# Kernel tuning notes

Measured on AMD Instinct MI355X. Metric: run time of the kernel, lower is better.

The kernel has to match this reference:

```python
import jax, jax.numpy as jnp
import numpy as np

N_EMBD = 2048
N_HEAD = 16
HEAD_DIM = N_EMBD // N_HEAD  # 128
ROPE_BASE = 10000.0


def _rope_cos_sin(T, dim, dtype):
    theta = 1.0 / (ROPE_BASE ** (jnp.arange(0, dim, 2, dtype=jnp.float32) / dim))  # [dim/2]
    freqs = jnp.arange(T, dtype=jnp.float32)[:, None] * theta[None, :]  # [T, dim/2]
    return jnp.cos(freqs).astype(dtype), jnp.sin(freqs).astype(dtype)


def _apply_rope(t, cos, sin):
    # t: [B,H,T,D]; interleaved (even, odd) pairs form complex numbers.
    B, H, T, D = t.shape
    tr = t.reshape(B, H, T, D // 2, 2)
    a, b = tr[..., 0], tr[..., 1]
    # (a + ib) * (cos + i sin)
    out = jnp.stack([a * cos - b * sin, a * sin + b * cos], axis=-1)
    return out.reshape(B, H, T, D)


def setup_inputs() -> dict:
    key = jax.random.key(0)
    k1, k2, k3 = jax.random.split(key, 3)
    B, T, C = 2, 2048, N_EMBD
    s = 1.0 / np.sqrt(C)
    return {
        "x": jax.random.normal(k1, (B, T, C), dtype=jnp.float32),
        "w_att": jax.random.normal(k2, (3 * C, C), dtype=jnp.float32) * s,
        "b_att": jnp.zeros((3 * C,), dtype=jnp.float32),
        "w_proj": jax.random.normal(k3, (C, C), dtype=jnp.float32) * s,
        "b_proj": jnp.zeros((C,), dtype=jnp.float32),
    }


def reference(x, w_att, b_att, w_proj, b_proj):
    B, T, C = x.shape
    H, D = N_HEAD, HEAD_DIM
    qkv = x @ w_att.T + b_att  # [B,T,3C]
    q, k, v = jnp.split(qkv, 3, axis=-1)
    # [B,T,C] -> [B,H,T,D]
    q, k, v = (t.reshape(B, T, H, D).transpose(0, 2, 1, 3) for t in (q, k, v))
    cos, sin = _rope_cos_sin(T, D, jnp.float32)  # [T, D/2]
    cos = cos[None, None]  # [1,1,T,D/2]
    sin = sin[None, None]
    q = _apply_rope(q, cos, sin)
    k = _apply_rope(k, cos, sin)
    # causal SDPA
    scale = 1.0 / np.sqrt(D)
    scores = jnp.einsum('bhqd,bhkd->bhqk', q, k) * scale
    mask = jnp.tril(jnp.ones((T, T), dtype=bool))
    scores = jnp.where(mask, scores, jnp.finfo(scores.dtype).min)
    attn = jax.nn.softmax(scores, axis=-1)
    y = jnp.einsum('bhqk,bhkd->bhqd', attn, v)  # [B,H,T,D]
    y = y.transpose(0, 2, 1, 3).reshape(B, T, C)
    return y @ w_proj.T + b_proj
```

## Files before the change

kernel.cpp:

```cpp
#include <hip/hip_runtime.h>
#include <hip/hip_bf16.h>
#include <math.h>

#define DEVI __device__ __forceinline__

typedef __attribute__((ext_vector_type(8))) short bf16x8;
typedef __attribute__((ext_vector_type(4))) float f32x4;

constexpr int Bn = 2;
constexpr int Tn = 2048;
constexpr int Cn = 2048;
constexpr int Hn = 16;
constexpr int Dn = 128;
constexpr int Mrows = Bn * Tn;
constexpr int Nqkv = 3 * Cn;
constexpr int BH = Bn * Hn;
constexpr int NKT = Cn / 32;

DEVI f32x4 mfma16x16(bf16x8 a, bf16x8 b, f32x4 c) {
    return __builtin_amdgcn_mfma_f32_16x16x32_bf16(a, b, c, 0, 0, 0);
}

DEVI bf16x8 load8(const __hip_bfloat16* p) {
    return *(const bf16x8*)p;
}

DEVI bf16x8 lds8c(const char* p, int byte_off) {
    return *(const bf16x8*)(p + byte_off);
}

DEVI short bf16bits(float f) {
    union { __hip_bfloat16 b; short s; } u;
    u.b = __float2bfloat16(f);
    return u.s;
}

typedef const __attribute__((address_space(1))) void* gas1_t;
typedef __attribute__((address_space(3))) void* las3_t;
DEVI void stage16(const __hip_bfloat16* g, __hip_bfloat16* l) {
    __builtin_amdgcn_global_load_lds((gas1_t)g, (las3_t)l, 16, 0, 0);
}

__global__ __launch_bounds__(256) void cvt_kernel(
    const float* __restrict__ src, __hip_bfloat16* __restrict__ dst)
{
    const size_t i8 = ((size_t)blockIdx.x * 256 + threadIdx.x) * 8;
    const float4 a = *(const float4*)(src + i8);
    const float4 b = *(const float4*)(src + i8 + 4);
    union { bf16x8 v; __hip_bfloat16 h[8]; } u;
    u.h[0] = __float2bfloat16(a.x); u.h[1] = __float2bfloat16(a.y);
    u.h[2] = __float2bfloat16(a.z); u.h[3] = __float2bfloat16(a.w);
    u.h[4] = __float2bfloat16(b.x); u.h[5] = __float2bfloat16(b.y);
    u.h[6] = __float2bfloat16(b.z); u.h[7] = __float2bfloat16(b.w);
    *(bf16x8*)(dst + i8) = u.v;
}

__global__ __launch_bounds__(256) void qkv_gemm_kernel(
    const __hip_bfloat16* __restrict__ xb,
    const __hip_bfloat16* __restrict__ wab,
    const float* __restrict__ bias,
    __hip_bfloat16* __restrict__ Qo,
    __hip_bfloat16* __restrict__ Ko,
    __hip_bfloat16* __restrict__ Vt)
{
    __shared__ __align__(16) __hip_bfloat16 As[2][128 * 32];
    __shared__ __align__(16) __hip_bfloat16 Bs[2][128 * 32];
    const int tid  = threadIdx.x;
    const int lane = tid & 63;
    const int wid  = tid >> 6;
    const int quad = lane >> 4;
    const int l16  = lane & 15;
    const int bm = blockIdx.y * 128;
    const int bn = blockIdx.x * 128;
    const int wm = (wid >> 1) * 64;
    const int wn = (wid & 1) * 64;

    const int lr = lane >> 2;
    const int lc = (lane & 3) * 8;
    const int r0 = 32 * wid;
    const __hip_bfloat16* Ag0 = xb  + (size_t)(bm + r0 + lr) * Cn + lc;
    const __hip_bfloat16* Ag1 = xb  + (size_t)(bm + r0 + 16 + lr) * Cn + lc;
    const __hip_bfloat16* Bg0 = wab + (size_t)(bn + r0 + lr) * Cn + lc;
    const __hip_bfloat16* Bg1 = wab + (size_t)(bn + r0 + 16 + lr) * Cn + lc;
    const int lbase0 = r0 * 32 + lane * 8;
    const int lbase1 = (r0 + 16) * 32 + lane * 8;

    const f32x4 zero = {0.f, 0.f, 0.f, 0.f};
    f32x4 acc[4][4];
#pragma unroll
    for (int i = 0; i < 4; ++i)
#pragma unroll
        for (int j = 0; j < 4; ++j) acc[i][j] = zero;

    stage16(Ag0, &As[0][lbase0]);
    stage16(Ag1, &As[0][lbase1]);
    stage16(Bg0, &Bs[0][lbase0]);
    stage16(Bg1, &Bs[0][lbase1]);
    __syncthreads();

    for (int kt = 0; kt < NKT; ++kt) {
        const int cur = kt & 1;
        if (kt + 1 < NKT) {
            const int kn = (kt + 1) * 32;
            stage16(Ag0 + kn, &As[cur ^ 1][lbase0]);
            stage16(Ag1 + kn, &As[cur ^ 1][lbase1]);
            stage16(Bg0 + kn, &Bs[cur ^ 1][lbase0]);
            stage16(Bg1 + kn, &Bs[cur ^ 1][lbase1]);
        }
        bf16x8 af[4], bfr[4];
#pragma unroll
        for (int i = 0; i < 4; ++i)
            af[i] = load8(&As[cur][(wm + i * 16 + l16) * 32 + quad * 8]);
#pragma unroll
        for (int j = 0; j < 4; ++j)
            bfr[j] = load8(&Bs[cur][(wn + j * 16 + l16) * 32 + quad * 8]);
#pragma unroll
        for (int i = 0; i < 4; ++i)
#pragma unroll
            for (int j = 0; j < 4; ++j)
                acc[i][j] = mfma16x16(af[i], bfr[j], acc[i][j]);
        __syncthreads();
    }

#pragma unroll
    for (int j = 0; j < 4; ++j) {
        const int n = bn + wn + j * 16 + l16;
        const float bv = bias[n];
        const int sel = n >> 11;
        const int c   = n & 2047;
        const int h   = c >> 7;
        const int d   = c & 127;
#pragma unroll
        for (int i = 0; i < 4; ++i) {
#pragma unroll
            for (int r = 0; r < 4; ++r) {
                const int m = bm + wm + i * 16 + quad * 4 + r;
                const int b = m >> 11;
                const int t = m & 2047;
                const int bh = b * Hn + h;
                const __hip_bfloat16 hv = __float2bfloat16(acc[i][j][r] + bv);
                if (sel == 0)      Qo[((size_t)bh * Tn + t) * Dn + d] = hv;
                else if (sel == 1) Ko[((size_t)bh * Tn + t) * Dn + d] = hv;
                else               Vt[((size_t)bh * Dn + d) * Tn + t] = hv;
            }
        }
    }
}

__global__ __launch_bounds__(256) void rope_kernel(
    __hip_bfloat16* __restrict__ Qo,
    __hip_bfloat16* __restrict__ Ko)
{
    const size_t idx = (size_t)blockIdx.x * blockDim.x + threadIdx.x;
    const int d2 = (int)(idx & 63);
    const int t  = (int)((idx >> 6) & (size_t)(Tn - 1));
    const float inv = exp2f(-(float)d2 * (1.0f / 64.0f) * 13.287712379549449f);
    float sn, cs;
    sincosf((float)t * inv, &sn, &cs);
    const size_t base = (idx >> 6) * (size_t)Dn + (size_t)(2 * d2);
    {
        const float a = __bfloat162float(Qo[base]);
        const float b = __bfloat162float(Qo[base + 1]);
        Qo[base]     = __float2bfloat16(a * cs - b * sn);
        Qo[base + 1] = __float2bfloat16(a * sn + b * cs);
    }
    {
        const float a = __bfloat162float(Ko[base]);
        const float b = __bfloat162float(Ko[base + 1]);
        Ko[base]     = __float2bfloat16(a * cs - b * sn);
        Ko[base + 1] = __float2bfloat16(a * sn + b * cs);
    }
}

__global__ __launch_bounds__(256) void flash_kernel(
    const __hip_bfloat16* __restrict__ Qo,
    const __hip_bfloat16* __restrict__ Ko,
    const __hip_bfloat16* __restrict__ Vt,
    __hip_bfloat16* __restrict__ Y)
{
    __shared__ __align__(16) short Ks[2][64 * 128];
    __shared__ __align__(16) short Vs[2][128 * 64];
    __shared__ __align__(16) short Ps[4][16 * 72];
    const int tid  = threadIdx.x;
    const int lane = tid & 63;
    const int wid  = tid >> 6;
    const int quad = lane >> 4;
    const int l16  = lane & 15;
    const int bh   = blockIdx.x & (BH - 1);
    const int qblk = 31 - (blockIdx.x >> 5);
    const int q0w  = qblk * 64 + wid * 16;
    const int nkt  = qblk + 1;

    const __hip_bfloat16* Qb = Qo + (size_t)bh * Tn * Dn;
    const __hip_bfloat16* Kg = Ko + (size_t)bh * Tn * Dn;
    const __hip_bfloat16* Vg = Vt + (size_t)bh * Dn * Tn;
    short* P = &Ps[wid][0];

    const int kr  = tid >> 4;
    const int ksl = (tid & 15) ^ kr;
    const __hip_bfloat16* KgA = Kg + (size_t)kr * Dn + ksl * 8;
    const int vr  = tid >> 3;
    const int vsl = (tid & 7) ^ (vr & 7);
    const __hip_bfloat16* VgA = Vg + (size_t)vr * Tn + vsl * 8;

    int koff[4];
#pragma unroll
    for (int ks = 0; ks < 4; ++ks)
        koff[ks] = l16 * 256 + ((((ks * 4 + quad) ^ l16) & 15) << 4);
    int vkey[2];
#pragma unroll
    for (int h = 0; h < 2; ++h)
        vkey[h] = (((h * 4 + quad) ^ (l16 & 7)) << 4);

    bf16x8 qf[4];
#pragma unroll
    for (int ks = 0; ks < 4; ++ks)
        qf[ks] = load8(Qb + (size_t)(q0w + l16) * Dn + ks * 32 + quad * 8);

    const f32x4 zero = {0.f, 0.f, 0.f, 0.f};
    f32x4 o[8];
#pragma unroll
    for (int j = 0; j < 8; ++j) o[j] = zero;
    float lpart[4] = {0.f, 0.f, 0.f, 0.f};
    const float scale2 = 0.12751743430267602f;

#pragma unroll
    for (int c = 0; c < 4; ++c) {
        stage16(KgA + (size_t)(c * 16) * Dn, (__hip_bfloat16*)&Ks[0][c * 2048 + tid * 8]);
        stage16(VgA + (size_t)(c * 32) * Tn, (__hip_bfloat16*)&Vs[0][c * 2048 + tid * 8]);
    }
    __syncthreads();

    for (int kt = 0; kt < nkt; ++kt) {
        const int cur = kt & 1;
        if (kt + 1 < nkt) {
            const int kb2 = (kt + 1) * 64;
            const int nxt = cur ^ 1;
#pragma unroll
            for (int c = 0; c < 4; ++c) {
                stage16(KgA + (size_t)(kb2 + c * 16) * Dn,
                        (__hip_bfloat16*)&Ks[nxt][c * 2048 + tid * 8]);
                stage16(VgA + (size_t)(c * 32) * Tn + kb2,
                        (__hip_bfloat16*)&Vs[nxt][c * 2048 + tid * 8]);
            }
        }
        const int kb = kt * 64;
        if (kb <= q0w + 15) {
            f32x4 sc[4];
#pragma unroll
            for (int g = 0; g < 4; ++g) sc[g] = zero;
#pragma unroll
            for (int ks = 0; ks < 4; ++ks) {
#pragma unroll
                for (int g = 0; g < 4; ++g) {
                    bf16x8 kf = lds8c((const char*)&Ks[cur][0], koff[ks] + g * 4096);
                    sc[g] = mfma16x16(qf[ks], kf, sc[g]);
                }
            }
            if (kb + 63 <= q0w) {
#pragma unroll
                for (int g = 0; g < 4; ++g)
#pragma unroll
                    for (int r = 0; r < 4; ++r) {
                        const float p = exp2f(sc[g][r] * scale2);
                        lpart[r] += p;
                        P[(quad * 4 + r) * 72 + g * 16 + l16] = bf16bits(p);
                    }
            } else {
#pragma unroll
                for (int g = 0; g < 4; ++g)
#pragma unroll
                    for (int r = 0; r < 4; ++r) {
                        const int row = q0w + quad * 4 + r;
                        const float a = (kb + g * 16 + l16 <= row)
                                        ? sc[g][r] * scale2 : -INFINITY;
                        const float p = exp2f(a);
                        lpart[r] += p;
                        P[(quad * 4 + r) * 72 + g * 16 + l16] = bf16bits(p);
                    }
            }
            __builtin_amdgcn_sched_barrier(0);
            bf16x8 af0 = *(const bf16x8*)(P + l16 * 72 + quad * 8);
            bf16x8 af1 = *(const bf16x8*)(P + l16 * 72 + 32 + quad * 8);
#pragma unroll
            for (int j = 0; j < 8; ++j) {
                bf16x8 vf0 = lds8c((const char*)&Vs[cur][0], (j * 16 + l16) * 128 + vkey[0]);
                bf16x8 vf1 = lds8c((const char*)&Vs[cur][0], (j * 16 + l16) * 128 + vkey[1]);
                o[j] = mfma16x16(af0, vf0, o[j]);
                o[j] = mfma16x16(af1, vf1, o[j]);
            }
            __builtin_amdgcn_sched_barrier(0);
        }
        __syncthreads();
    }

    float invl[4];
#pragma unroll
    for (int r = 0; r < 4; ++r) {
        float s = lpart[r];
#pragma unroll
        for (int off = 1; off < 16; off <<= 1)
            s += __shfl_xor(s, off, 16);
        invl[r] = 1.0f / s;
    }

    const int b = bh >> 4;
    const int h = bh & 15;
#pragma unroll
    for (int j = 0; j < 8; ++j) {
#pragma unroll
        for (int r = 0; r < 4; ++r) {
            const int t = q0w + quad * 4 + r;
            Y[((size_t)b * Tn + t) * Cn + h * Dn + j * 16 + l16] =
                __float2bfloat16(o[j][r] * invl[r]);
        }
    }
}

__global__ __launch_bounds__(256) void proj_gemm_kernel(
    const __hip_bfloat16* __restrict__ Yb,
    const __hip_bfloat16* __restrict__ wpb,
    const float* __restrict__ bias,
    float* __restrict__ out)
{
    __shared__ __align__(16) __hip_bfloat16 As[2][128 * 32];
    __shared__ __align__(16) __hip_bfloat16 Bs[2][128 * 32];
    const int tid  = threadIdx.x;
    const int lane = tid & 63;
    const int wid  = tid >> 6;
    const int quad = lane >> 4;
    const int l16  = lane & 15;
    const int bm = blockIdx.y * 128;
    const int bn = blockIdx.x * 128;
    const int wm = (wid >> 1) * 64;
    const int wn = (wid & 1) * 64;

    const int lr = lane >> 2;
    const int lc = (lane & 3) * 8;
    const int r0 = 32 * wid;
    const __hip_bfloat16* Ag0 = Yb  + (size_t)(bm + r0 + lr) * Cn + lc;
    const __hip_bfloat16* Ag1 = Yb  + (size_t)(bm + r0 + 16 + lr) * Cn + lc;
    const __hip_bfloat16* Bg0 = wpb + (size_t)(bn + r0 + lr) * Cn + lc;
    const __hip_bfloat16* Bg1 = wpb + (size_t)(bn + r0 + 16 + lr) * Cn + lc;
    const int lbase0 = r0 * 32 + lane * 8;
    const int lbase1 = (r0 + 16) * 32 + lane * 8;

    const f32x4 zero = {0.f, 0.f, 0.f, 0.f};
    f32x4 acc[4][4];
#pragma unroll
    for (int i = 0; i < 4; ++i)
#pragma unroll
        for (int j = 0; j < 4; ++j) acc[i][j] = zero;

    stage16(Ag0, &As[0][lbase0]);
    stage16(Ag1, &As[0][lbase1]);
    stage16(Bg0, &Bs[0][lbase0]);
    stage16(Bg1, &Bs[0][lbase1]);
    __syncthreads();

    for (int kt = 0; kt < NKT; ++kt) {
        const int cur = kt & 1;
        if (kt + 1 < NKT) {
            const int kn = (kt + 1) * 32;
            stage16(Ag0 + kn, &As[cur ^ 1][lbase0]);
            stage16(Ag1 + kn, &As[cur ^ 1][lbase1]);
            stage16(Bg0 + kn, &Bs[cur ^ 1][lbase0]);
            stage16(Bg1 + kn, &Bs[cur ^ 1][lbase1]);
        }
        bf16x8 af[4], bfr[4];
#pragma unroll
        for (int i = 0; i < 4; ++i)
            af[i] = load8(&As[cur][(wm + i * 16 + l16) * 32 + quad * 8]);
#pragma unroll
        for (int j = 0; j < 4; ++j)
            bfr[j] = load8(&Bs[cur][(wn + j * 16 + l16) * 32 + quad * 8]);
#pragma unroll
        for (int i = 0; i < 4; ++i)
#pragma unroll
            for (int j = 0; j < 4; ++j)
                acc[i][j] = mfma16x16(af[i], bfr[j], acc[i][j]);
        __syncthreads();
    }

#pragma unroll
    for (int j = 0; j < 4; ++j) {
        const int n = bn + wn + j * 16 + l16;
        const float bv = bias[n];
#pragma unroll
        for (int i = 0; i < 4; ++i) {
#pragma unroll
            for (int r = 0; r < 4; ++r) {
                const int m = bm + wm + i * 16 + quad * 4 + r;
                out[(size_t)m * Cn + n] = acc[i][j][r] + bv;
            }
        }
    }
}

extern "C" void kernel_launch(void* const* d_in, const int* in_sizes, int n_in,
                              void* d_out, int out_size, void* d_ws, size_t ws_size,
                              hipStream_t stream)
{
    const float* x      = (const float*)d_in[0];
    const float* w_att  = (const float*)d_in[1];
    const float* b_att  = (const float*)d_in[2];
    const float* w_proj = (const float*)d_in[3];
    const float* b_proj = (const float*)d_in[4];
    float* out = (float*)d_out;

    const size_t per  = (size_t)BH * Tn * Dn;
    const size_t wabN = (size_t)Nqkv * Cn;
    __hip_bfloat16* Qo  = (__hip_bfloat16*)d_ws;
    __hip_bfloat16* Ko  = Qo + per;
    __hip_bfloat16* Vt  = Ko + per;
    __hip_bfloat16* xb  = Vt + per;
    __hip_bfloat16* wab = xb + per;
    __hip_bfloat16* wpb = wab + wabN;
    __hip_bfloat16* Yb  = xb;

    dim3 blk(256);
    cvt_kernel<<<dim3((Mrows * Cn) / 2048), blk, 0, stream>>>(x, xb);
    cvt_kernel<<<dim3((Nqkv * Cn) / 2048), blk, 0, stream>>>(w_att, wab);
    cvt_kernel<<<dim3((Cn * Cn) / 2048), blk, 0, stream>>>(w_proj, wpb);
    qkv_gemm_kernel<<<dim3(Nqkv / 128, Mrows / 128), blk, 0, stream>>>(
        xb, wab, b_att, Qo, Ko, Vt);
    rope_kernel<<<dim3((BH * Tn * 64) / 256), blk, 0, stream>>>(Qo, Ko);
    flash_kernel<<<dim3((Tn / 64) * BH), blk, 0, stream>>>(Qo, Ko, Vt, Yb);
    proj_gemm_kernel<<<dim3(Cn / 128, Mrows / 128), blk, 0, stream>>>(
        Yb, wpb, b_proj, out);
}
```

Before: 420.7 us.

## Double per-warp query rows in flash kernel and fuse the three conversion launches

The flash attention kernel now gives each warp two 16-row query fragments, so each block covers 128 query rows. Every staged K/V tile and every K fragment read from LDS now feeds twice as many MFMAs, and the grid is halved. The causal schedule pairs the long and short query blocks, and launch bounds request two blocks per SM. The three fp32-to-bf16 conversion kernels become one launch that picks its source array by index, which saves launch overhead. The costs are higher register pressure from the doubled accumulators, and a shared P buffer that is reused back to back across the two fragments.

```diff
diff --git a/kernel.cpp b/kernel.cpp
--- a/kernel.cpp
+++ b/kernel.cpp
@@ -41,12 +41,20 @@
     __builtin_amdgcn_global_load_lds((gas1_t)g, (las3_t)l, 16, 0, 0);
 }
 
-__global__ __launch_bounds__(256) void cvt_kernel(
-    const float* __restrict__ src, __hip_bfloat16* __restrict__ dst)
+__global__ __launch_bounds__(256) void cvt3_kernel(
+    const float* __restrict__ s0,
+    const float* __restrict__ s1,
+    const float* __restrict__ s2,
+    __hip_bfloat16* __restrict__ dst,
+    long n0, long n1)
 {
     const size_t i8 = ((size_t)blockIdx.x * 256 + threadIdx.x) * 8;
-    const float4 a = *(const float4*)(src + i8);
-    const float4 b = *(const float4*)(src + i8 + 4);
+    const float* src;
+    if ((long)i8 < n0)            src = s0 + i8;
+    else if ((long)i8 < n0 + n1)  src = s1 + (i8 - n0);
+    else                          src = s2 + (i8 - n0 - n1);
+    const float4 a = *(const float4*)(src);
+    const float4 b = *(const float4*)(src + 4);
     union { bf16x8 v; __hip_bfloat16 h[8]; } u;
     u.h[0] = __float2bfloat16(a.x); u.h[1] = __float2bfloat16(a.y);
     u.h[2] = __float2bfloat16(a.z); u.h[3] = __float2bfloat16(a.w);
@@ -172,7 +180,7 @@
     }
 }
 
-__global__ __launch_bounds__(256) void flash_kernel(
+__global__ __launch_bounds__(256, 2) void flash_kernel(
     const __hip_bfloat16* __restrict__ Qo,
     const __hip_bfloat16* __restrict__ Ko,
     const __hip_bfloat16* __restrict__ Vt,
@@ -187,9 +195,10 @@
     const int quad = lane >> 4;
     const int l16  = lane & 15;
     const int bh   = blockIdx.x & (BH - 1);
-    const int qblk = 31 - (blockIdx.x >> 5);
-    const int q0w  = qblk * 64 + wid * 16;
-    const int nkt  = qblk + 1;
+    const int g    = blockIdx.x >> 5;
+    const int qblk = (g < 8) ? (15 - g) : (g - 8);
+    const int q0w  = qblk * 128 + wid * 32;
+    const int nkt  = 2 * qblk + 2;
 
     const __hip_bfloat16* Qb = Qo + (size_t)bh * Tn * Dn;
     const __hip_bfloat16* Kg = Ko + (size_t)bh * Tn * Dn;
@@ -212,16 +221,20 @@
     for (int h = 0; h < 2; ++h)
         vkey[h] = (((h * 4 + quad) ^ (l16 & 7)) << 4);
 
-    bf16x8 qf[4];
-#pragma unroll
-    for (int ks = 0; ks < 4; ++ks)
-        qf[ks] = load8(Qb + (size_t)(q0w + l16) * Dn + ks * 32 + quad * 8);
+    bf16x8 qf[2][4];
+#pragma unroll
+    for (int f = 0; f < 2; ++f)
+#pragma unroll
+        for (int ks = 0; ks < 4; ++ks)
+            qf[f][ks] = load8(Qb + (size_t)(q0w + f * 16 + l16) * Dn + ks * 32 + quad * 8);
 
     const f32x4 zero = {0.f, 0.f, 0.f, 0.f};
-    f32x4 o[8];
-#pragma unroll
-    for (int j = 0; j < 8; ++j) o[j] = zero;
-    float lpart[4] = {0.f, 0.f, 0.f, 0.f};
+    f32x4 o[2][8];
+#pragma unroll
+    for (int f = 0; f < 2; ++f)
+#pragma unroll
+        for (int j = 0; j < 8; ++j) o[f][j] = zero;
+    float lpart[2][4] = {{0.f, 0.f, 0.f, 0.f}, {0.f, 0.f, 0.f, 0.f}};
     const float scale2 = 0.12751743430267602f;
 
 #pragma unroll
@@ -245,74 +258,83 @@
             }
         }
         const int kb = kt * 64;
-        if (kb <= q0w + 15) {
-            f32x4 sc[4];
-#pragma unroll
-            for (int g = 0; g < 4; ++g) sc[g] = zero;
+        if (kb <= q0w + 31) {
+            f32x4 sc[2][4];
+#pragma unroll
+            for (int f = 0; f < 2; ++f)
+#pragma unroll
+                for (int gg = 0; gg < 4; ++gg) sc[f][gg] = zero;
 #pragma unroll
             for (int ks = 0; ks < 4; ++ks) {
 #pragma unroll
-                for (int g = 0; g < 4; ++g) {
-                    bf16x8 kf = lds8c((const char*)&Ks[cur][0], koff[ks] + g * 4096);
-                    sc[g] = mfma16x16(qf[ks], kf, sc[g]);
+                for (int gg = 0; gg < 4; ++gg) {
+                    bf16x8 kf = lds8c((const char*)&Ks[cur][0], koff[ks] + gg * 4096);
+                    sc[0][gg] = mfma16x16(qf[0][ks], kf, sc[0][gg]);
+                    sc[1][gg] = mfma16x16(qf[1][ks], kf, sc[1][gg]);
                 }
             }
-            if (kb + 63 <= q0w) {
-#pragma unroll
-                for (int g = 0; g < 4; ++g)
-#pragma unroll
-                    for (int r = 0; r < 4; ++r) {
-                        const float p = exp2f(sc[g][r] * scale2);
-                        lpart[r] += p;
-                        P[(quad * 4 + r) * 72 + g * 16 + l16] = bf16bits(p);
-                    }
-            } else {
-#pragma unroll
-                for (int g = 0; g < 4; ++g)
-#pragma unroll
-                    for (int r = 0; r < 4; ++r) {
-                        const int row = q0w + quad * 4 + r;
-                        const float a = (kb + g * 16 + l16 <= row)
-                                        ? sc[g][r] * scale2 : -INFINITY;
-                        const float p = exp2f(a);
-                        lpart[r] += p;
-                        P[(quad * 4 + r) * 72 + g * 16 + l16] = bf16bits(p);
-                    }
-            }
-            __builtin_amdgcn_sched_barrier(0);
-            bf16x8 af0 = *(const bf16x8*)(P + l16 * 72 + quad * 8);
-            bf16x8 af1 = *(const bf16x8*)(P + l16 * 72 + 32 + quad * 8);
-#pragma unroll
-            for (int j = 0; j < 8; ++j) {
-                bf16x8 vf0 = lds8c((const char*)&Vs[cur][0], (j * 16 + l16) * 128 + vkey[0]);
-                bf16x8 vf1 = lds8c((const char*)&Vs[cur][0], (j * 16 + l16) * 128 + vkey[1]);
-                o[j] = mfma16x16(af0, vf0, o[j]);
-                o[j] = mfma16x16(af1, vf1, o[j]);
-            }
-            __builtin_amdgcn_sched_barrier(0);
+#pragma unroll
+            for (int f = 0; f < 2; ++f) {
+                const int rowbase = q0w + f * 16;
+                if (kb + 63 <= rowbase) {
+#pragma unroll
+                    for (int gg = 0; gg < 4; ++gg)
+#pragma unroll
+                        for (int r = 0; r < 4; ++r) {
+                            const float p = exp2f(sc[f][gg][r] * scale2);
+                            lpart[f][r] += p;
+                            P[(quad * 4 + r) * 72 + gg * 16 + l16] = bf16bits(p);
+                        }
+                } else {
+#pragma unroll
+                    for (int gg = 0; gg < 4; ++gg)
+#pragma unroll
+                        for (int r = 0; r < 4; ++r) {
+                            const int row = rowbase + quad * 4 + r;
+                            const float a = (kb + gg * 16 + l16 <= row)
+                                            ? sc[f][gg][r] * scale2 : -INFINITY;
+                            const float p = exp2f(a);
+                            lpart[f][r] += p;
+                            P[(quad * 4 + r) * 72 + gg * 16 + l16] = bf16bits(p);
+                        }
+                }
+                __builtin_amdgcn_sched_barrier(0);
+                bf16x8 af0 = *(const bf16x8*)(P + l16 * 72 + quad * 8);
+                bf16x8 af1 = *(const bf16x8*)(P + l16 * 72 + 32 + quad * 8);
+#pragma unroll
+                for (int j = 0; j < 8; ++j) {
+                    bf16x8 vf0 = lds8c((const char*)&Vs[cur][0], (j * 16 + l16) * 128 + vkey[0]);
+                    bf16x8 vf1 = lds8c((const char*)&Vs[cur][0], (j * 16 + l16) * 128 + vkey[1]);
+                    o[f][j] = mfma16x16(af0, vf0, o[f][j]);
+                    o[f][j] = mfma16x16(af1, vf1, o[f][j]);
+                }
+                __builtin_amdgcn_sched_barrier(0);
+            }
         }
         __syncthreads();
-    }
-
-    float invl[4];
-#pragma unroll
-    for (int r = 0; r < 4; ++r) {
-        float s = lpart[r];
-#pragma unroll
-        for (int off = 1; off < 16; off <<= 1)
-            s += __shfl_xor(s, off, 16);
-        invl[r] = 1.0f / s;
     }
 
     const int b = bh >> 4;
     const int h = bh & 15;
 #pragma unroll
-    for (int j = 0; j < 8; ++j) {
+    for (int f = 0; f < 2; ++f) {
+        float invl[4];
 #pragma unroll
         for (int r = 0; r < 4; ++r) {
-            const int t = q0w + quad * 4 + r;
-            Y[((size_t)b * Tn + t) * Cn + h * Dn + j * 16 + l16] =
-                __float2bfloat16(o[j][r] * invl[r]);
+            float s = lpart[f][r];
+#pragma unroll
+            for (int off = 1; off < 16; off <<= 1)
+                s += __shfl_xor(s, off, 16);
+            invl[r] = 1.0f / s;
+        }
+#pragma unroll
+        for (int j = 0; j < 8; ++j) {
+#pragma unroll
+            for (int r = 0; r < 4; ++r) {
+                const int t = q0w + f * 16 + quad * 4 + r;
+                Y[((size_t)b * Tn + t) * Cn + h * Dn + j * 16 + l16] =
+                    __float2bfloat16(o[f][j][r] * invl[r]);
+            }
         }
     }
 }
@@ -418,14 +440,17 @@
     __hip_bfloat16* wpb = wab + wabN;
     __hip_bfloat16* Yb  = xb;
 
+    const long n0 = (long)Mrows * Cn;
+    const long n1 = (long)Nqkv * Cn;
+    const long n2 = (long)Cn * Cn;
+
     dim3 blk(256);
-    cvt_kernel<<<dim3((Mrows * Cn) / 2048), blk, 0, stream>>>(x, xb);
-    cvt_kernel<<<dim3((Nqkv * Cn) / 2048), blk, 0, stream>>>(w_att, wab);
-    cvt_kernel<<<dim3((Cn * Cn) / 2048), blk, 0, stream>>>(w_proj, wpb);
+    cvt3_kernel<<<dim3((unsigned)((n0 + n1 + n2) / 2048)), blk, 0, stream>>>(
+        x, w_att, w_proj, xb, n0, n1);
     qkv_gemm_kernel<<<dim3(Nqkv / 128, Mrows / 128), blk, 0, stream>>>(
         xb, wab, b_att, Qo, Ko, Vt);
     rope_kernel<<<dim3((BH * Tn * 64) / 256), blk, 0, stream>>>(Qo, Ko);
-    flash_kernel<<<dim3((Tn / 64) * BH), blk, 0, stream>>>(Qo, Ko, Vt, Yb);
+    flash_kernel<<<dim3((Tn / 128) * BH), blk, 0, stream>>>(Qo, Ko, Vt, Yb);
     proj_gemm_kernel<<<dim3(Cn / 128, Mrows / 128), blk, 0, stream>>>(
         Yb, wpb, b_proj, out);
 }
```

Result: no change. 428.4 us (+1.8%).
